# Kernel tuning notes

Measured on AMD Instinct MI355X. Metric: run time of the kernel, lower is better.

Reference implementation:

```python
import jax, jax.numpy as jnp
import numpy as np
import math

NUM_HEADS = 16
HEAD_DIM = 64


def _apply_rope(x, sin2, cos2):
    # x: [B,H,S,D]; sin2/cos2: [1,1,S,D] interleaved-duplicated sin/cos
    x_even = x[..., ::2]
    x_odd = x[..., 1::2]
    rot = jnp.stack([-x_odd, x_even], axis=-1).reshape(x.shape)
    return x * cos2 + rot * sin2


def setup_inputs() -> dict:
    key = jax.random.key(0)
    k1, k2, k3, k4 = jax.random.split(key, 4)
    B, S, D = 2, 2048, 1024
    hidden_states = jax.random.normal(k1, (B, S, D), dtype=jnp.float32)
    # RoFormer-style sinusoidal_pos: first half sin, second half cos
    half = HEAD_DIM // 2
    inv_freq = 1.0 / (10000.0 ** (np.arange(0, half, dtype=np.float32) / half))
    t = np.arange(S, dtype=np.float32)
    ang = np.einsum('s,d->sd', t, inv_freq)  # [S, half]
    sinusoidal_pos = jnp.asarray(
        np.concatenate([np.sin(ang), np.cos(ang)], axis=-1)[None, None]
    )  # [1,1,S,HEAD_DIM]
    attention_mask = jnp.zeros((B, 1, 1, S), dtype=jnp.float32)
    scale = 0.02
    Wq = jax.random.normal(k2, (D, D), dtype=jnp.float32) * scale
    Wk = jax.random.normal(k3, (D, D), dtype=jnp.float32) * scale
    Wv = jax.random.normal(k4, (D, D), dtype=jnp.float32) * scale
    return {
        'hidden_states': hidden_states,
        'sinusoidal_pos': sinusoidal_pos,
        'attention_mask': attention_mask,
        'Wq': Wq,
        'Wk': Wk,
        'Wv': Wv,
    }


def reference(hidden_states, sinusoidal_pos, attention_mask, Wq, Wk, Wv):
    B, S, D = hidden_states.shape
    H, Dh = NUM_HEADS, HEAD_DIM

    def split_heads(x):  # [B,S,D] -> [B,H,S,Dh]
        return x.reshape(B, S, H, Dh).transpose(0, 2, 1, 3)

    q = split_heads(hidden_states @ Wq.T)
    k = split_heads(hidden_states @ Wk.T)
    v = split_heads(hidden_states @ Wv.T)

    # sinusoidal_pos: [1,1,S,Dh]; chunk -> sin, cos halves, then interleave-duplicate
    sin, cos = jnp.split(sinusoidal_pos, 2, axis=-1)
    sin2 = jnp.repeat(sin, 2, axis=-1)
    cos2 = jnp.repeat(cos, 2, axis=-1)
    q = _apply_rope(q, sin2, cos2)
    k = _apply_rope(k, sin2, cos2)

    scores = jnp.einsum('bhqd,bhkd->bhqk', q, k) / math.sqrt(Dh)
    scores = scores + attention_mask  # additive mask broadcasts over heads/query
    probs = jax.nn.softmax(scores, axis=-1)
    ctx = jnp.einsum('bhqk,bhkd->bhqd', probs, v)
    ctx = ctx.transpose(0, 2, 1, 3).reshape(B, S, D)
    return ctx
```

## Files before the change

### kernel.cpp

```cpp
#include <hip/hip_runtime.h>
#include <math.h>

#define B_  2
#define S_  2048
#define D_  1024
#define H_  16
#define DH  64
#define M_  (B_*S_)
#define QKSZ 4194304

typedef __attribute__((ext_vector_type(4)))  float  f32x4;
typedef __attribute__((ext_vector_type(16))) float  f32x16;
typedef __attribute__((ext_vector_type(8)))  short  short8;
typedef __attribute__((ext_vector_type(8)))  unsigned short ushort8;
typedef __attribute__((ext_vector_type(4)))  unsigned short us4;

static __device__ __forceinline__ unsigned short f2bf(float x) {
    union { float f; unsigned int u; } v; v.f = x;
    unsigned int u = v.u;
    u += 0x7fffu + ((u >> 16) & 1u);
    return (unsigned short)(u >> 16);
}

__global__ __launch_bounds__(256) void qkv_proj(
    const float* __restrict__ hid,
    const float* __restrict__ sp,
    const float* __restrict__ Wq,
    const float* __restrict__ Wk,
    const float* __restrict__ Wv,
    unsigned short* __restrict__ qk_ws,
    unsigned short* __restrict__ vt_ws)
{
    __shared__ unsigned short As[128 * 32];
    __shared__ unsigned short Bs[128 * 32];

    const int tid    = threadIdx.x;
    const int tile_m = (blockIdx.x & 31) * 128;
    const int tile_n = (blockIdx.x >> 5) * 128;

    const float* W; int nloc;
    if (tile_n < 1024)      { W = Wq; nloc = tile_n; }
    else if (tile_n < 2048) { W = Wk; nloc = tile_n - 1024; }
    else                    { W = Wv; nloc = tile_n - 2048; }

    const int w    = tid >> 6, lane = tid & 63;
    const int wr   = w >> 1,  wc   = w & 1;
    const int g    = lane >> 4, c16 = lane & 15;
    const int srow = tid >> 3;
    const int scol = (tid & 7) * 4;

    f32x4 acc[4][4];
    #pragma unroll
    for (int i = 0; i < 4; ++i)
        #pragma unroll
        for (int j = 0; j < 4; ++j)
            acc[i][j][0] = acc[i][j][1] = acc[i][j][2] = acc[i][j][3] = 0.f;

    for (int k0 = 0; k0 < 1024; k0 += 32) {
        #pragma unroll
        for (int p = 0; p < 4; ++p) {
            const int row = p * 32 + srow;
            float4 a = *(const float4*)&hid[(size_t)(tile_m + row) * 1024 + k0 + scol];
            float4 b = *(const float4*)&W  [(size_t)(nloc   + row) * 1024 + k0 + scol];
            us4 ap, bp;
            ap[0] = f2bf(a.x); ap[1] = f2bf(a.y); ap[2] = f2bf(a.z); ap[3] = f2bf(a.w);
            bp[0] = f2bf(b.x); bp[1] = f2bf(b.y); bp[2] = f2bf(b.z); bp[3] = f2bf(b.w);
            *(us4*)&As[p * 1024 + tid * 4] = ap;
            *(us4*)&Bs[p * 1024 + tid * 4] = bp;
        }
        __syncthreads();

        short8 af[4], bf[4];
        #pragma unroll
        for (int i = 0; i < 4; ++i)
            af[i] = *(const short8*)&As[(wr * 64 + i * 16 + c16) * 32 + g * 8];
        #pragma unroll
        for (int j = 0; j < 4; ++j)
            bf[j] = *(const short8*)&Bs[(wc * 64 + j * 16 + c16) * 32 + g * 8];
        #pragma unroll
        for (int i = 0; i < 4; ++i)
            #pragma unroll
            for (int j = 0; j < 4; ++j)
                acc[i][j] = __builtin_amdgcn_mfma_f32_16x16x32_bf16(
                    af[i], bf[j], acc[i][j], 0, 0, 0);
        __syncthreads();
    }

    if (tile_n < 2048) {
        const int isK = (tile_n >= 1024) ? 1 : 0;
        unsigned short* qkb = qk_ws + (size_t)isK * QKSZ;
        const int head = ((tile_n - (isK ? 1024 : 0)) + wc * 64) >> 6;
        #pragma unroll
        for (int j = 0; j < 4; ++j) {
            const int dh = j * 16 + c16;
            const int p  = dh >> 1;
            const int odd = dh & 1;
            #pragma unroll
            for (int i = 0; i < 4; ++i) {
                #pragma unroll
                for (int r = 0; r < 4; ++r) {
                    const int m = tile_m + wr * 64 + i * 16 + 4 * g + r;
                    const int b = m >> 11, s = m & 2047;
                    float v    = acc[i][j][r];
                    float part = __shfl_xor(v, 1);
                    float sv = sp[s * 64 + p];
                    float cv = sp[s * 64 + 32 + p];
                    float o  = odd ? (v * cv + part * sv) : (v * cv - part * sv);
                    qkb[((size_t)(b * H_ + head) * S_ + s) * DH + dh] = f2bf(o);
                }
            }
        }
    } else {
        const int head = (tile_n - 2048 + wc * 64) >> 6;
        #pragma unroll
        for (int j = 0; j < 4; ++j) {
            const int dh = j * 16 + c16;
            #pragma unroll
            for (int i = 0; i < 4; ++i) {
                const int m0 = tile_m + wr * 64 + i * 16 + 4 * g;
                const int b = m0 >> 11, s0 = m0 & 2047;
                us4 o;
                o[0] = f2bf(acc[i][j][0]); o[1] = f2bf(acc[i][j][1]);
                o[2] = f2bf(acc[i][j][2]); o[3] = f2bf(acc[i][j][3]);
                *(us4*)&vt_ws[((size_t)(b * H_ + head) * DH + dh) * S_ + s0] = o;
            }
        }
    }
}

__global__ __launch_bounds__(256, 2) void attn_fwd(
    const unsigned short* __restrict__ qk_ws,
    const unsigned short* __restrict__ vt_ws,
    const float* __restrict__ maskp,
    float* __restrict__ out)
{
    __shared__ unsigned short K_lds[2][64 * 64];
    __shared__ unsigned short V_lds[2][64 * 64];

    const int tid  = threadIdx.x;
    const int w    = tid >> 6, lane = tid & 63;
    const int hi   = lane >> 5, c32 = lane & 31;
    const int qt   = blockIdx.x & 15;
    const int bh   = blockIdx.x >> 4;
    const int b    = bh >> 4, h = bh & 15;

    const unsigned short* qp = qk_ws + (size_t)bh * (S_ * DH);
    const unsigned short* kp = qk_ws + QKSZ + (size_t)bh * (S_ * DH);
    const unsigned short* vp = vt_ws + (size_t)bh * (DH * S_);
    const float* mp = maskp + b * S_;

    const int q = qt * 128 + w * 32 + c32;

    short8 qf[4];
    #pragma unroll
    for (int ks = 0; ks < 4; ++ks)
        qf[ks] = *(const short8*)&qp[(size_t)q * DH + ks * 16 + 8 * hi];

    f32x16 ctx[2];
    #pragma unroll
    for (int d = 0; d < 2; ++d)
        #pragma unroll
        for (int r = 0; r < 16; ++r) ctx[d][r] = 0.f;
    float mrow = -1e30f, lsum = 0.f;

    ushort8 rk[2], rv[2];
    const int su0 = tid, su1 = tid + 256;

    auto LOADT = [&](int t) {
        const int kv = t * 64;
        {
            int row = su0 >> 3, c = (su0 & 7) * 8;
            rk[0] = *(const ushort8*)&kp[(size_t)(kv + row) * DH + c];
            rv[0] = *(const ushort8*)&vp[(size_t)row * S_ + kv + c];
        }
        {
            int row = su1 >> 3, c = (su1 & 7) * 8;
            rk[1] = *(const ushort8*)&kp[(size_t)(kv + row) * DH + c];
            rv[1] = *(const ushort8*)&vp[(size_t)row * S_ + kv + c];
        }
    };
    auto WRITET = [&](int buf) {
        {
            int row = su0 >> 3, c = (su0 & 7) * 16;
            int off = (row * 128 + c) ^ ((row & 7) << 4);
            *(ushort8*)((char*)&K_lds[buf][0] + off) = rk[0];
            *(ushort8*)((char*)&V_lds[buf][0] + off) = rv[0];
        }
        {
            int row = su1 >> 3, c = (su1 & 7) * 16;
            int off = (row * 128 + c) ^ ((row & 7) << 4);
            *(ushort8*)((char*)&K_lds[buf][0] + off) = rk[1];
            *(ushort8*)((char*)&V_lds[buf][0] + off) = rv[1];
        }
    };

    LOADT(0); WRITET(0); LOADT(1);
    __syncthreads();

    const int NT = S_ / 64;
    for (int t = 0; t < NT; ++t) {
        const int cur = t & 1;
        const int kv  = t * 64;
        const char* Kb = (const char*)&K_lds[cur][0];
        const char* Vb = (const char*)&V_lds[cur][0];

        f32x16 sa0, sa1;
        #pragma unroll
        for (int r = 0; r < 16; ++r) { sa0[r] = 0.f; sa1[r] = 0.f; }
        #pragma unroll
        for (int ks = 0; ks < 4; ++ks) {
            const int colb = ks * 32 + hi * 16;
            short8 kf0 = *(const short8*)(Kb + ((c32 * 128 + colb) ^ ((c32 & 7) << 4)));
            short8 kf1 = *(const short8*)(Kb + (((32 + c32) * 128 + colb) ^ ((c32 & 7) << 4)));
            sa0 = __builtin_amdgcn_mfma_f32_32x32x16_bf16(kf0, qf[ks], sa0, 0, 0, 0);
            sa1 = __builtin_amdgcn_mfma_f32_32x32x16_bf16(kf1, qf[ks], sa1, 0, 0, 0);
        }

        float sc0[16], sc1[16];
        #pragma unroll
        for (int r = 0; r < 16; ++r) {
            const int koff = (r & 3) + 8 * (r >> 2) + 4 * hi;
            sc0[r] = sa0[r] * 0.125f + mp[kv + koff];
            sc1[r] = sa1[r] * 0.125f + mp[kv + 32 + koff];
        }

        float pm = sc0[0];
        #pragma unroll
        for (int r = 1; r < 16; ++r) pm = fmaxf(pm, sc0[r]);
        #pragma unroll
        for (int r = 0; r < 16; ++r) pm = fmaxf(pm, sc1[r]);
        pm = fmaxf(pm, __shfl_xor(pm, 32));

        const float mnew = fmaxf(mrow, pm);
        const float fac  = __expf(mrow - mnew);
        mrow = mnew;
        lsum *= fac;
        #pragma unroll
        for (int d = 0; d < 2; ++d)
            #pragma unroll
            for (int r = 0; r < 16; ++r) ctx[d][r] *= fac;

        float p0[16], p1[16];
        float ps = 0.f;
        #pragma unroll
        for (int r = 0; r < 16; ++r) { p0[r] = __expf(sc0[r] - mnew); ps += p0[r]; }
        #pragma unroll
        for (int r = 0; r < 16; ++r) { p1[r] = __expf(sc1[r] - mnew); ps += p1[r]; }
        lsum += ps;

        short8 pf[4];
        #pragma unroll
        for (int ks4 = 0; ks4 < 4; ++ks4) {
            const float* pp = (ks4 < 2) ? p0 : p1;
            const int k8 = (ks4 & 1) * 8;
            unsigned int a0 = ((unsigned int)f2bf(pp[k8 + 1]) << 16) | f2bf(pp[k8 + 0]);
            unsigned int a1 = ((unsigned int)f2bf(pp[k8 + 3]) << 16) | f2bf(pp[k8 + 2]);
            unsigned int b0 = ((unsigned int)f2bf(pp[k8 + 5]) << 16) | f2bf(pp[k8 + 4]);
            unsigned int b1 = ((unsigned int)f2bf(pp[k8 + 7]) << 16) | f2bf(pp[k8 + 6]);
            unsigned int ax0 = (unsigned int)__shfl_xor((int)a0, 32);
            unsigned int ax1 = (unsigned int)__shfl_xor((int)a1, 32);
            unsigned int bx0 = (unsigned int)__shfl_xor((int)b0, 32);
            unsigned int bx1 = (unsigned int)__shfl_xor((int)b1, 32);
            union { unsigned int u[4]; short8 v; } fr;
            fr.u[0] = hi ? bx0 : a0;
            fr.u[1] = hi ? bx1 : a1;
            fr.u[2] = hi ? b0  : ax0;
            fr.u[3] = hi ? b1  : ax1;
            pf[ks4] = fr.v;
        }

        if (t + 1 < NT) {
            __syncthreads();
            WRITET(cur ^ 1);
            if (t + 2 < NT) LOADT(t + 2);
        }

        #pragma unroll
        for (int ks4 = 0; ks4 < 4; ++ks4) {
            const int colb = ks4 * 32 + hi * 16;
            short8 vf0 = *(const short8*)(Vb + ((c32 * 128 + colb) ^ ((c32 & 7) << 4)));
            short8 vf1 = *(const short8*)(Vb + (((32 + c32) * 128 + colb) ^ ((c32 & 7) << 4)));
            ctx[0] = __builtin_amdgcn_mfma_f32_32x32x16_bf16(vf0, pf[ks4], ctx[0], 0, 0, 0);
            ctx[1] = __builtin_amdgcn_mfma_f32_32x32x16_bf16(vf1, pf[ks4], ctx[1], 0, 0, 0);
        }

        if (t + 1 < NT) __syncthreads();
    }

    const float inv = 1.0f / (lsum + __shfl_xor(lsum, 32));

    float* ob = out + ((size_t)(b * S_ + q) * D_) + h * DH;
    #pragma unroll
    for (int d = 0; d < 2; ++d)
        #pragma unroll
        for (int q4 = 0; q4 < 4; ++q4) {
            f32x4 st;
            st[0] = ctx[d][q4 * 4 + 0] * inv;
            st[1] = ctx[d][q4 * 4 + 1] * inv;
            st[2] = ctx[d][q4 * 4 + 2] * inv;
            st[3] = ctx[d][q4 * 4 + 3] * inv;
            *(f32x4*)&ob[d * 32 + 8 * q4 + 4 * hi] = st;
        }
}

extern "C" void kernel_launch(void* const* d_in, const int* in_sizes, int n_in,
                              void* d_out, int out_size, void* d_ws, size_t ws_size,
                              hipStream_t stream) {
    (void)in_sizes; (void)n_in; (void)out_size; (void)ws_size;
    const float* hid  = (const float*)d_in[0];
    const float* sp   = (const float*)d_in[1];
    const float* mask = (const float*)d_in[2];
    const float* Wq   = (const float*)d_in[3];
    const float* Wk   = (const float*)d_in[4];
    const float* Wv   = (const float*)d_in[5];
    float* out = (float*)d_out;

    unsigned short* qk_ws = (unsigned short*)d_ws;
    unsigned short* vt_ws = qk_ws + 2 * (size_t)QKSZ;

    qkv_proj<<<dim3(32 * 24), dim3(256), 0, stream>>>(hid, sp, Wq, Wk, Wv, qk_ws, vt_ws);
    attn_fwd<<<dim3(32 * 16), dim3(256), 0, stream>>>(qk_ws, vt_ws, mask, out);
}
```

Baseline: 229.0 us.

## Pre-convert inputs to bf16, use direct global-to-LDS loads, lazy softmax rescale

Adds a separate pass that converts hidden states and the weights to bf16 in workspace. The GEMM then streams these bf16 tiles straight into LDS with global_load_lds instead of loading fp32 and converting per tile. It also raises wave priority around the MFMA blocks and skips the online-softmax rescale unless the running max grows by more than 8. This cuts redundant conversion and register traffic in the GEMM, but adds an extra kernel launch and extra memory round trips, and falls back to the old path if the workspace is too small.

```diff
diff --git a/kernel.cpp b/kernel.cpp
--- a/kernel.cpp
+++ b/kernel.cpp
@@ -22,12 +22,39 @@
     return (unsigned short)(u >> 16);
 }
 
-__global__ __launch_bounds__(256) void qkv_proj(
-    const float* __restrict__ hid,
+typedef __attribute__((address_space(3))) void       lds_void;
+typedef const __attribute__((address_space(1))) void gbl_void;
+
+static __device__ __forceinline__ void gload_lds16(const unsigned short* g,
+                                                   unsigned short* l) {
+    __builtin_amdgcn_global_load_lds((gbl_void*)g, (lds_void*)l, 16, 0, 0);
+}
+
+__global__ __launch_bounds__(256) void cvt_all(
+    const float* __restrict__ hid, const float* __restrict__ Wq,
+    const float* __restrict__ Wk,  const float* __restrict__ Wv,
+    unsigned short* __restrict__ hb, unsigned short* __restrict__ wb)
+{
+    const size_t i = ((size_t)blockIdx.x * 256 + threadIdx.x) * 8;
+    const float* s; unsigned short* d;
+    if (i < 4194304) { s = hid + i; d = hb + i; }
+    else {
+        size_t j = i - 4194304;
+        const float* w = (j < 1048576) ? Wq : (j < 2097152) ? Wk : Wv;
+        s = w + (j & 1048575);
+        d = wb + j;
+    }
+    float4 a = *(const float4*)s, b = *(const float4*)(s + 4);
+    ushort8 o;
+    o[0] = f2bf(a.x); o[1] = f2bf(a.y); o[2] = f2bf(a.z); o[3] = f2bf(a.w);
+    o[4] = f2bf(b.x); o[5] = f2bf(b.y); o[6] = f2bf(b.z); o[7] = f2bf(b.w);
+    *(ushort8*)d = o;
+}
+
+__global__ __launch_bounds__(256) void qkv_gemm(
+    const unsigned short* __restrict__ hb,
+    const unsigned short* __restrict__ wb,
     const float* __restrict__ sp,
-    const float* __restrict__ Wq,
-    const float* __restrict__ Wk,
-    const float* __restrict__ Wv,
     unsigned short* __restrict__ qk_ws,
     unsigned short* __restrict__ vt_ws)
 {
@@ -38,16 +65,18 @@
     const int tile_m = (blockIdx.x & 31) * 128;
     const int tile_n = (blockIdx.x >> 5) * 128;
 
-    const float* W; int nloc;
-    if (tile_n < 1024)      { W = Wq; nloc = tile_n; }
-    else if (tile_n < 2048) { W = Wk; nloc = tile_n - 1024; }
-    else                    { W = Wv; nloc = tile_n - 2048; }
-
-    const int w    = tid >> 6, lane = tid & 63;
-    const int wr   = w >> 1,  wc   = w & 1;
-    const int g    = lane >> 4, c16 = lane & 15;
-    const int srow = tid >> 3;
-    const int scol = (tid & 7) * 4;
+    const int w  = tid >> 6, lane = tid & 63;
+    const int wr = w >> 1,  wc = w & 1;
+    const int g  = lane >> 4, c16 = lane & 15;
+    const int lr = lane >> 2;
+    const int lc = (lane & 3) * 8;
+
+    const size_t arow = (size_t)(tile_m + w * 16 + lr) * 1024 + lc;
+    const size_t brow = (size_t)(tile_n + w * 16 + lr) * 1024 + lc;
+    unsigned short* lA0 = &As[(w * 16) * 32];
+    unsigned short* lA1 = &As[(w * 16 + 64) * 32];
+    unsigned short* lB0 = &Bs[(w * 16) * 32];
+    unsigned short* lB1 = &Bs[(w * 16 + 64) * 32];
 
     f32x4 acc[4][4];
     #pragma unroll
@@ -57,17 +86,10 @@
             acc[i][j][0] = acc[i][j][1] = acc[i][j][2] = acc[i][j][3] = 0.f;
 
     for (int k0 = 0; k0 < 1024; k0 += 32) {
-        #pragma unroll
-        for (int p = 0; p < 4; ++p) {
-            const int row = p * 32 + srow;
-            float4 a = *(const float4*)&hid[(size_t)(tile_m + row) * 1024 + k0 + scol];
-            float4 b = *(const float4*)&W  [(size_t)(nloc   + row) * 1024 + k0 + scol];
-            us4 ap, bp;
-            ap[0] = f2bf(a.x); ap[1] = f2bf(a.y); ap[2] = f2bf(a.z); ap[3] = f2bf(a.w);
-            bp[0] = f2bf(b.x); bp[1] = f2bf(b.y); bp[2] = f2bf(b.z); bp[3] = f2bf(b.w);
-            *(us4*)&As[p * 1024 + tid * 4] = ap;
-            *(us4*)&Bs[p * 1024 + tid * 4] = bp;
-        }
+        gload_lds16(hb + arow + k0,             lA0);
+        gload_lds16(hb + arow + 64 * 1024 + k0, lA1);
+        gload_lds16(wb + brow + k0,             lB0);
+        gload_lds16(wb + brow + 64 * 1024 + k0, lB1);
         __syncthreads();
 
         short8 af[4], bf[4];
@@ -77,12 +99,14 @@
         #pragma unroll
         for (int j = 0; j < 4; ++j)
             bf[j] = *(const short8*)&Bs[(wc * 64 + j * 16 + c16) * 32 + g * 8];
+        __builtin_amdgcn_s_setprio(1);
         #pragma unroll
         for (int i = 0; i < 4; ++i)
             #pragma unroll
             for (int j = 0; j < 4; ++j)
                 acc[i][j] = __builtin_amdgcn_mfma_f32_16x16x32_bf16(
                     af[i], bf[j], acc[i][j], 0, 0, 0);
+        __builtin_amdgcn_s_setprio(0);
         __syncthreads();
     }
 
@@ -128,6 +152,112 @@
     }
 }
 
+__global__ __launch_bounds__(256) void qkv_proj(
+    const float* __restrict__ hid,
+    const float* __restrict__ sp,
+    const float* __restrict__ Wq,
+    const float* __restrict__ Wk,
+    const float* __restrict__ Wv,
+    unsigned short* __restrict__ qk_ws,
+    unsigned short* __restrict__ vt_ws)
+{
+    __shared__ unsigned short As[128 * 32];
+    __shared__ unsigned short Bs[128 * 32];
+
+    const int tid    = threadIdx.x;
+    const int tile_m = (blockIdx.x & 31) * 128;
+    const int tile_n = (blockIdx.x >> 5) * 128;
+
+    const float* W; int nloc;
+    if (tile_n < 1024)      { W = Wq; nloc = tile_n; }
+    else if (tile_n < 2048) { W = Wk; nloc = tile_n - 1024; }
+    else                    { W = Wv; nloc = tile_n - 2048; }
+
+    const int w    = tid >> 6, lane = tid & 63;
+    const int wr   = w >> 1,  wc   = w & 1;
+    const int g    = lane >> 4, c16 = lane & 15;
+    const int srow = tid >> 3;
+    const int scol = (tid & 7) * 4;
+
+    f32x4 acc[4][4];
+    #pragma unroll
+    for (int i = 0; i < 4; ++i)
+        #pragma unroll
+        for (int j = 0; j < 4; ++j)
+            acc[i][j][0] = acc[i][j][1] = acc[i][j][2] = acc[i][j][3] = 0.f;
+
+    for (int k0 = 0; k0 < 1024; k0 += 32) {
+        #pragma unroll
+        for (int p = 0; p < 4; ++p) {
+            const int row = p * 32 + srow;
+            float4 a = *(const float4*)&hid[(size_t)(tile_m + row) * 1024 + k0 + scol];
+            float4 b = *(const float4*)&W  [(size_t)(nloc   + row) * 1024 + k0 + scol];
+            us4 ap, bp;
+            ap[0] = f2bf(a.x); ap[1] = f2bf(a.y); ap[2] = f2bf(a.z); ap[3] = f2bf(a.w);
+            bp[0] = f2bf(b.x); bp[1] = f2bf(b.y); bp[2] = f2bf(b.z); bp[3] = f2bf(b.w);
+            *(us4*)&As[p * 1024 + tid * 4] = ap;
+            *(us4*)&Bs[p * 1024 + tid * 4] = bp;
+        }
+        __syncthreads();
+
+        short8 af[4], bf[4];
+        #pragma unroll
+        for (int i = 0; i < 4; ++i)
+            af[i] = *(const short8*)&As[(wr * 64 + i * 16 + c16) * 32 + g * 8];
+        #pragma unroll
+        for (int j = 0; j < 4; ++j)
+            bf[j] = *(const short8*)&Bs[(wc * 64 + j * 16 + c16) * 32 + g * 8];
+        #pragma unroll
+        for (int i = 0; i < 4; ++i)
+            #pragma unroll
+            for (int j = 0; j < 4; ++j)
+                acc[i][j] = __builtin_amdgcn_mfma_f32_16x16x32_bf16(
+                    af[i], bf[j], acc[i][j], 0, 0, 0);
+        __syncthreads();
+    }
+
+    if (tile_n < 2048) {
+        const int isK = (tile_n >= 1024) ? 1 : 0;
+        unsigned short* qkb = qk_ws + (size_t)isK * QKSZ;
+        const int head = ((tile_n - (isK ? 1024 : 0)) + wc * 64) >> 6;
+        #pragma unroll
+        for (int j = 0; j < 4; ++j) {
+            const int dh = j * 16 + c16;
+            const int p  = dh >> 1;
+            const int odd = dh & 1;
+            #pragma unroll
+            for (int i = 0; i < 4; ++i) {
+                #pragma unroll
+                for (int r = 0; r < 4; ++r) {
+                    const int m = tile_m + wr * 64 + i * 16 + 4 * g + r;
+                    const int b = m >> 11, s = m & 2047;
+                    float v    = acc[i][j][r];
+                    float part = __shfl_xor(v, 1);
+                    float sv = sp[s * 64 + p];
+                    float cv = sp[s * 64 + 32 + p];
+                    float o  = odd ? (v * cv + part * sv) : (v * cv - part * sv);
+                    qkb[((size_t)(b * H_ + head) * S_ + s) * DH + dh] = f2bf(o);
+                }
+            }
+        }
+    } else {
+        const int head = (tile_n - 2048 + wc * 64) >> 6;
+        #pragma unroll
+        for (int j = 0; j < 4; ++j) {
+            const int dh = j * 16 + c16;
+            #pragma unroll
+            for (int i = 0; i < 4; ++i) {
+                const int m0 = tile_m + wr * 64 + i * 16 + 4 * g;
+                const int b = m0 >> 11, s0 = m0 & 2047;
+                us4 o;
+                o[0] = f2bf(acc[i][j][0]); o[1] = f2bf(acc[i][j][1]);
+                o[2] = f2bf(acc[i][j][2]); o[3] = f2bf(acc[i][j][3]);
+                *(us4*)&vt_ws[((size_t)(b * H_ + head) * DH + dh) * S_ + s0] = o;
+            }
+        }
+    }
+}
+
 __global__ __launch_bounds__(256, 2) void attn_fwd(
     const unsigned short* __restrict__ qk_ws,
     const unsigned short* __restrict__ vt_ws,
@@ -207,6 +337,7 @@
         f32x16 sa0, sa1;
         #pragma unroll
         for (int r = 0; r < 16; ++r) { sa0[r] = 0.f; sa1[r] = 0.f; }
+        __builtin_amdgcn_s_setprio(1);
         #pragma unroll
         for (int ks = 0; ks < 4; ++ks) {
             const int colb = ks * 32 + hi * 16;
@@ -215,6 +346,7 @@
             sa0 = __builtin_amdgcn_mfma_f32_32x32x16_bf16(kf0, qf[ks], sa0, 0, 0, 0);
             sa1 = __builtin_amdgcn_mfma_f32_32x32x16_bf16(kf1, qf[ks], sa1, 0, 0, 0);
         }
+        __builtin_amdgcn_s_setprio(0);
 
         float sc0[16], sc1[16];
         #pragma unroll
@@ -231,21 +363,23 @@
         for (int r = 0; r < 16; ++r) pm = fmaxf(pm, sc1[r]);
         pm = fmaxf(pm, __shfl_xor(pm, 32));
 
-        const float mnew = fmaxf(mrow, pm);
-        const float fac  = __expf(mrow - mnew);
-        mrow = mnew;
-        lsum *= fac;
-        #pragma unroll
-        for (int d = 0; d < 2; ++d)
-            #pragma unroll
-            for (int r = 0; r < 16; ++r) ctx[d][r] *= fac;
+        if (!__all(pm - mrow <= 8.0f)) {
+            const float mnew = fmaxf(mrow, pm);
+            const float fac  = __expf(mrow - mnew);
+            mrow = mnew;
+            lsum *= fac;
+            #pragma unroll
+            for (int d = 0; d < 2; ++d)
+                #pragma unroll
+                for (int r = 0; r < 16; ++r) ctx[d][r] *= fac;
+        }
 
         float p0[16], p1[16];
         float ps = 0.f;
         #pragma unroll
-        for (int r = 0; r < 16; ++r) { p0[r] = __expf(sc0[r] - mnew); ps += p0[r]; }
-        #pragma unroll
-        for (int r = 0; r < 16; ++r) { p1[r] = __expf(sc1[r] - mnew); ps += p1[r]; }
+        for (int r = 0; r < 16; ++r) { p0[r] = __expf(sc0[r] - mrow); ps += p0[r]; }
+        #pragma unroll
+        for (int r = 0; r < 16; ++r) { p1[r] = __expf(sc1[r] - mrow); ps += p1[r]; }
         lsum += ps;
 
         short8 pf[4];
@@ -275,6 +409,7 @@
             if (t + 2 < NT) LOADT(t + 2);
         }
 
+        __builtin_amdgcn_s_setprio(1);
         #pragma unroll
         for (int ks4 = 0; ks4 < 4; ++ks4) {
             const int colb = ks4 * 32 + hi * 16;
@@ -283,6 +418,7 @@
             ctx[0] = __builtin_amdgcn_mfma_f32_32x32x16_bf16(vf0, pf[ks4], ctx[0], 0, 0, 0);
             ctx[1] = __builtin_amdgcn_mfma_f32_32x32x16_bf16(vf1, pf[ks4], ctx[1], 0, 0, 0);
         }
+        __builtin_amdgcn_s_setprio(0);
 
         if (t + 1 < NT) __syncthreads();
     }
@@ -306,7 +442,7 @@
 extern "C" void kernel_launch(void* const* d_in, const int* in_sizes, int n_in,
                               void* d_out, int out_size, void* d_ws, size_t ws_size,
                               hipStream_t stream) {
-    (void)in_sizes; (void)n_in; (void)out_size; (void)ws_size;
+    (void)in_sizes; (void)n_in; (void)out_size;
     const float* hid  = (const float*)d_in[0];
     const float* sp   = (const float*)d_in[1];
     const float* mask = (const float*)d_in[2];
@@ -317,7 +453,15 @@
 
     unsigned short* qk_ws = (unsigned short*)d_ws;
     unsigned short* vt_ws = qk_ws + 2 * (size_t)QKSZ;
-
-    qkv_proj<<<dim3(32 * 24), dim3(256), 0, stream>>>(hid, sp, Wq, Wk, Wv, qk_ws, vt_ws);
+    unsigned short* hb    = vt_ws + (size_t)QKSZ;
+    unsigned short* wb    = hb + 4194304;
+
+    const size_t NEED = 39845888;
+    if (ws_size >= NEED) {
+        cvt_all<<<dim3(3584), dim3(256), 0, stream>>>(hid, Wq, Wk, Wv, hb, wb);
+        qkv_gemm<<<dim3(32 * 24), dim3(256), 0, stream>>>(hb, wb, sp, qk_ws, vt_ws);
+    } else {
+        qkv_proj<<<dim3(32 * 24), dim3(256), 0, stream>>>(hid, sp, Wq, Wk, Wv, qk_ws, vt_ws);
+    }
     attn_fwd<<<dim3(32 * 16), dim3(256), 0, stream>>>(qk_ws, vt_ws, mask, out);
 }
```

After: 197.2 us. -13.9%, faster.
